# Kernel tuning notes

Hardware: AMD Instinct MI355X
Metric: run time of the kernel (lower is better)

The kernel has to match this reference:

```python
import jax, jax.numpy as jnp
import numpy as np

B, L, HID = 256, 4096, 128
INNER = 8
LR = 0.01  # INFERENCE_LR


def setup_inputs() -> dict:
    key = jax.random.key(0)
    k_h, k_w1, k_b1, k_w2, k_b2 = jax.random.split(key, 5)
    bound1 = 1.0 / np.sqrt(HID)
    bound2 = 1.0 / np.sqrt(INNER)
    return {
        "h": jax.random.normal(k_h, (B, L, HID), dtype=jnp.float32),
        "W1": jax.random.uniform(k_w1, (INNER, HID), jnp.float32, -bound1, bound1),
        "b1": jax.random.uniform(k_b1, (INNER,), jnp.float32, -bound1, bound1),
        "W2": jax.random.uniform(k_w2, (HID, INNER), jnp.float32, -bound2, bound2),
        "b2": jax.random.uniform(k_b2, (HID,), jnp.float32, -bound2, bound2),
    }


def reference(h, W1, b1, W2, b2):
    Bsz, Ls, H = h.shape
    ts = jnp.arange(0, Ls - 3, 2)  # SGD step positions (static)
    inv_h = 2.0 / H  # d(mean sq err)/d(pred) factor over H elements

    def per_batch(hb):  # hb: (L, H)
        ks = hb[ts]       # keys  h[b, t]
        vs = hb[ts + 1]   # values h[b, t+1]

        def step(carry, kv):
            w1, c1, w2, c2 = carry
            k, v = kv
            a = w1 @ k + c1                 # (inner,)
            r = jnp.maximum(a, 0.0)
            pred = w2 @ r + c2              # (H,)
            g = inv_h * (pred - v)          # dLoss/dpred
            dW2 = jnp.outer(g, r)
            db2 = g
            da = (w2.T @ g) * (a > 0)
            dW1 = jnp.outer(da, k)
            db1 = da
            return (w1 - LR * dW1, c1 - LR * db1,
                    w2 - LR * dW2, c2 - LR * db2), None

        (w1, c1, w2, c2), _ = jax.lax.scan(step, (W1, b1, W2, b2), (ks, vs))
        x = hb[-1]
        return w2 @ jnp.maximum(w1 @ x + c1, 0.0) + c2  # (H,)

    return jax.vmap(per_batch)(h)  # (B, H)
```

## Files before the change

kernel.cpp:

```cpp
#include <hip/hip_runtime.h>

#define LRC 0.01f
#define LSEQ 4096
#define HIDDIM 128

typedef float f32x2 __attribute__((ext_vector_type(2)));
typedef unsigned int u32x2 __attribute__((ext_vector_type(2)));

#define RL(x, L) __int_as_float(__builtin_amdgcn_readlane(__float_as_int(x), (L)))
#define RORADD(x, ctrl)                                                      \
  x += __int_as_float(__builtin_amdgcn_update_dpp(                           \
      0, __float_as_int(x), (ctrl), 0xf, 0xf, true))

__device__ __forceinline__ float allred4(float x0, float x1, float x2,
                                         float x3) {
  u32x2 s1 = __builtin_amdgcn_permlane32_swap(__float_as_uint(x0),
                                              __float_as_uint(x1), false, false);
  float z01 = __uint_as_float(s1.x) + __uint_as_float(s1.y);
  u32x2 s2 = __builtin_amdgcn_permlane32_swap(__float_as_uint(x2),
                                              __float_as_uint(x3), false, false);
  float z23 = __uint_as_float(s2.x) + __uint_as_float(s2.y);
  u32x2 s3 = __builtin_amdgcn_permlane16_swap(__float_as_uint(z01),
                                              __float_as_uint(z23), false, false);
  float y = __uint_as_float(s3.x) + __uint_as_float(s3.y);
  RORADD(y, 0x128); RORADD(y, 0x124); RORADD(y, 0x122); RORADD(y, 0x121);
  return y;
}

__device__ __forceinline__ float allred1(float x) {
  u32x2 s1 = __builtin_amdgcn_permlane32_swap(__float_as_uint(x),
                                              __float_as_uint(x), false, false);
  float z = __uint_as_float(s1.x) + __uint_as_float(s1.y);
  u32x2 s2 = __builtin_amdgcn_permlane16_swap(__float_as_uint(z),
                                              __float_as_uint(z), false, false);
  z = __uint_as_float(s2.x) + __uint_as_float(s2.y);
  RORADD(z, 0x128); RORADD(z, 0x124); RORADD(z, 0x122); RORADD(z, 0x121);
  return z;
}

#define BAR() asm volatile("s_waitcnt lgkmcnt(0)\n\ts_barrier" ::: "memory")

__global__ __launch_bounds__(128) void ttt_kernel(
    const float* __restrict__ h, const float* __restrict__ W1,
    const float* __restrict__ b1, const float* __restrict__ W2,
    const float* __restrict__ b2, float* __restrict__ out) {
  __shared__ __align__(16) float sm[80];
  const int b = blockIdx.x;
  const int tid = threadIdx.x;
  const int wv = tid >> 6;
  const int lane = tid & 63;
  const int g = lane >> 4;
  const int sig = ((g & 1) << 1) | (g >> 1);
  const int d0 = lane * 2;
  const float* __restrict__ hb = h + (size_t)b * (LSEQ * HIDDIM);

  if (wv == 0) {
    const float cneg = -(LRC * 2.0f / (float)HIDDIM);
    f32x2 w2v[8];
#pragma unroll
    for (int i = 0; i < 8; ++i) {
      w2v[i].x = W2[(size_t)d0 * 8 + i];
      w2v[i].y = W2[(size_t)(d0 + 1) * 8 + i];
    }
    f32x2 b2v = *(const f32x2*)(b2 + d0);
    float b1A = b1[sig], b1B = b1[4 + sig];
    f32x2 vS0 = *(const f32x2*)(hb + 1 * HIDDIM + d0);
    f32x2 vS1 = *(const f32x2*)(hb + 3 * HIDDIM + d0);
    f32x2 vS2 = *(const f32x2*)(hb + 5 * HIDDIM + d0);
    f32x2 vS3 = *(const f32x2*)(hb + 7 * HIDDIM + d0);
    float pGlx = 0.0f, pGly = 0.0f;
    float pR0 = 0, pR1 = 0, pR2 = 0, pR3 = 0, pR4 = 0, pR5 = 0, pR6 = 0,
          pR7 = 0;
    float dm2A = 0, dm2B = 0, dm1A = 0, dm1B = 0;

    BAR();

    auto CORE = [&](float aA, float aB, f32x2 vcur, float& daAo, float& daBo,
                    bool defer) {
      float rA = fmaxf(aA, 0.0f), rB = fmaxf(aB, 0.0f);
      float r0 = RL(rA, 0), r1 = RL(rA, 32), r2 = RL(rA, 16), r3 = RL(rA, 48);
      float r4 = RL(rB, 0), r5 = RL(rB, 32), r6 = RL(rB, 16), r7 = RL(rB, 48);
      float px0 = fmaf(w2v[0].x, r0, b2v.x), py0 = fmaf(w2v[0].y, r0, b2v.y);
      float px1 = w2v[1].x * r1, py1 = w2v[1].y * r1;
      px0 = fmaf(w2v[2].x, r2, px0); py0 = fmaf(w2v[2].y, r2, py0);
      px1 = fmaf(w2v[3].x, r3, px1); py1 = fmaf(w2v[3].y, r3, py1);
      px0 = fmaf(w2v[4].x, r4, px0); py0 = fmaf(w2v[4].y, r4, py0);
      px1 = fmaf(w2v[5].x, r5, px1); py1 = fmaf(w2v[5].y, r5, py1);
      px0 = fmaf(w2v[6].x, r6, px0); py0 = fmaf(w2v[6].y, r6, py0);
      px1 = fmaf(w2v[7].x, r7, px1); py1 = fmaf(w2v[7].y, r7, py1);
      float glx = (px0 + px1 - vcur.x) * cneg;
      float gly = (py0 + py1 - vcur.y) * cneg;
      float dp[8];
#pragma unroll
      for (int i = 0; i < 8; ++i) dp[i] = fmaf(w2v[i].x, glx, w2v[i].y * gly);
      float zA = allred4(dp[0], dp[1], dp[2], dp[3]);
      float zB = allred4(dp[4], dp[5], dp[6], dp[7]);
      daAo = (aA > 0.0f) ? zA : 0.0f;
      daBo = (aB > 0.0f) ? zB : 0.0f;
      if (!defer) {
        w2v[0].x = fmaf(glx, r0, w2v[0].x); w2v[0].y = fmaf(gly, r0, w2v[0].y);
        w2v[1].x = fmaf(glx, r1, w2v[1].x); w2v[1].y = fmaf(gly, r1, w2v[1].y);
        w2v[2].x = fmaf(glx, r2, w2v[2].x); w2v[2].y = fmaf(gly, r2, w2v[2].y);
        w2v[3].x = fmaf(glx, r3, w2v[3].x); w2v[3].y = fmaf(gly, r3, w2v[3].y);
        w2v[4].x = fmaf(glx, r4, w2v[4].x); w2v[4].y = fmaf(gly, r4, w2v[4].y);
        w2v[5].x = fmaf(glx, r5, w2v[5].x); w2v[5].y = fmaf(gly, r5, w2v[5].y);
        w2v[6].x = fmaf(glx, r6, w2v[6].x); w2v[6].y = fmaf(gly, r6, w2v[6].y);
        w2v[7].x = fmaf(glx, r7, w2v[7].x); w2v[7].y = fmaf(gly, r7, w2v[7].y);
        b2v.x += glx;
        b2v.y += gly;
      } else {
        pGlx = glx; pGly = gly;
        pR0 = r0; pR1 = r1; pR2 = r2; pR3 = r3;
        pR4 = r4; pR5 = r5; pR6 = r6; pR7 = r7;
      }
    };

    auto APPLY_PEND = [&]() {
      w2v[0].x = fmaf(pGlx, pR0, w2v[0].x); w2v[0].y = fmaf(pGly, pR0, w2v[0].y);
      w2v[1].x = fmaf(pGlx, pR1, w2v[1].x); w2v[1].y = fmaf(pGly, pR1, w2v[1].y);
      w2v[2].x = fmaf(pGlx, pR2, w2v[2].x); w2v[2].y = fmaf(pGly, pR2, w2v[2].y);
      w2v[3].x = fmaf(pGlx, pR3, w2v[3].x); w2v[3].y = fmaf(pGly, pR3, w2v[3].y);
      w2v[4].x = fmaf(pGlx, pR4, w2v[4].x); w2v[4].y = fmaf(pGly, pR4, w2v[4].y);
      w2v[5].x = fmaf(pGlx, pR5, w2v[5].x); w2v[5].y = fmaf(pGly, pR5, w2v[5].y);
      w2v[6].x = fmaf(pGlx, pR6, w2v[6].x); w2v[6].y = fmaf(pGly, pR6, w2v[6].y);
      w2v[7].x = fmaf(pGlx, pR7, w2v[7].x); w2v[7].y = fmaf(pGly, pR7, w2v[7].y);
      b2v.x += pGlx;
      b2v.y += pGly;
    };

    auto EPA = [&](int ep, int e) {
      const int tpo = ep * 16, kko = 32 + ep * 5, dao = 48 + ep * 16;
      int rv0 = 4 * e + 9;  if (rv0 > 4095) rv0 = 4095;
      int rv1 = 4 * e + 11; if (rv1 > 4095) rv1 = 4095;
      f32x2 vI0 = *(const f32x2*)(hb + (size_t)rv0 * HIDDIM + d0);
      f32x2 vI1 = *(const f32x2*)(hb + (size_t)rv1 * HIDDIM + d0);
      float tpPA = sm[tpo + sig], tpPB = sm[tpo + 4 + sig];
      float tpQA = sm[tpo + 8 + sig], tpQB = sm[tpo + 12 + sig];
      float kk1 = sm[kko], kk2 = sm[kko + 1], kk3 = sm[kko + 2],
            kk4 = sm[kko + 3], kk5 = sm[kko + 4];
      APPLY_PEND();
      float aA = fmaf(dm2A, kk1, fmaf(dm1A, kk2, tpPA + b1A));
      float aB = fmaf(dm2B, kk1, fmaf(dm1B, kk2, tpPB + b1B));
      float daPA, daPB;
      CORE(aA, aB, vS0, daPA, daPB, false);
      if ((lane & 15) == 0) { sm[dao + sig] = daPA; sm[dao + 4 + sig] = daPB; }
      b1A += daPA;
      b1B += daPB;
      float aQA = fmaf(dm2A, kk3, fmaf(dm1A, kk4, fmaf(daPA, kk5, tpQA + b1A)));
      float aQB = fmaf(dm2B, kk3, fmaf(dm1B, kk4, fmaf(daPB, kk5, tpQB + b1B)));
      float daQA, daQB;
      CORE(aQA, aQB, vS1, daQA, daQB, true);
      if ((lane & 15) == 0) { sm[dao + 8 + sig] = daQA; sm[dao + 12 + sig] = daQB; }
      b1A += daQA;
      b1B += daQB;
      dm2A = daPA; dm2B = daPB;
      dm1A = daQA; dm1B = daQB;
      vS0 = vS2; vS1 = vS3; vS2 = vI0; vS3 = vI1;
      BAR();
    };

    for (int pr = 0; pr < 511; ++pr) {
      EPA(0, 2 * pr);
      EPA(1, 2 * pr + 1);
    }
    EPA(0, 1022);
    {
      float tpPA = sm[16 + sig], tpPB = sm[20 + sig];
      float tpQA = sm[24 + sig], tpQB = sm[28 + sig];
      float kk1 = sm[37], kk2 = sm[38], kk3 = sm[39], kk4 = sm[40],
            kk5 = sm[41];
      APPLY_PEND();
      float aA = fmaf(dm2A, kk1, fmaf(dm1A, kk2, tpPA + b1A));
      float aB = fmaf(dm2B, kk1, fmaf(dm1B, kk2, tpPB + b1B));
      float daA, daB;
      CORE(aA, aB, vS0, daA, daB, false);
      b1A += daA;
      b1B += daB;
      float fA = fmaf(dm2A, kk3, fmaf(dm1A, kk4, fmaf(daA, kk5, tpQA + b1A)));
      float fB = fmaf(dm2B, kk3, fmaf(dm1B, kk4, fmaf(daB, kk5, tpQB + b1B)));
      float rA = fmaxf(fA, 0.0f), rB = fmaxf(fB, 0.0f);
      float r0 = RL(rA, 0), r1 = RL(rA, 32), r2 = RL(rA, 16), r3 = RL(rA, 48);
      float r4 = RL(rB, 0), r5 = RL(rB, 32), r6 = RL(rB, 16), r7 = RL(rB, 48);
      float ox = fmaf(w2v[0].x, r0, b2v.x), oy = fmaf(w2v[0].y, r0, b2v.y);
      ox = fmaf(w2v[1].x, r1, ox); oy = fmaf(w2v[1].y, r1, oy);
      ox = fmaf(w2v[2].x, r2, ox); oy = fmaf(w2v[2].y, r2, oy);
      ox = fmaf(w2v[3].x, r3, ox); oy = fmaf(w2v[3].y, r3, oy);
      ox = fmaf(w2v[4].x, r4, ox); oy = fmaf(w2v[4].y, r4, oy);
      ox = fmaf(w2v[5].x, r5, ox); oy = fmaf(w2v[5].y, r5, oy);
      ox = fmaf(w2v[6].x, r6, ox); oy = fmaf(w2v[6].y, r6, oy);
      ox = fmaf(w2v[7].x, r7, ox); oy = fmaf(w2v[7].y, r7, oy);
      f32x2 o = {ox, oy};
      *(f32x2*)(out + (size_t)b * HIDDIM + d0) = o;
    }
  } else {
    f32x2 w1v[8];
#pragma unroll
    for (int i = 0; i < 8; ++i)
      w1v[i] = *(const f32x2*)(W1 + i * HIDDIM + d0);
    f32x2 kR2 = *(const f32x2*)(hb + 0 * HIDDIM + d0);
    f32x2 kR3 = *(const f32x2*)(hb + 2 * HIDDIM + d0);
    f32x2 kR4 = *(const f32x2*)(hb + 4 * HIDDIM + d0);
    f32x2 kR5 = *(const f32x2*)(hb + 6 * HIDDIM + d0);
    f32x2 kR0 = kR2, kR1 = kR2;
    f32x2 kI0 = *(const f32x2*)(hb + 8 * HIDDIM + d0);
    f32x2 kI1 = *(const f32x2*)(hb + 10 * HIDDIM + d0);
    if (lane < 16) sm[64 + lane] = 0.0f;
    {
      float pa[8], pb[8];
#pragma unroll
      for (int i = 0; i < 8; ++i) {
        pa[i] = fmaf(w1v[i].x, kR2.x, w1v[i].y * kR2.y);
        pb[i] = fmaf(w1v[i].x, kR3.x, w1v[i].y * kR3.y);
      }
      float zA = allred4(pa[0], pa[1], pa[2], pa[3]);
      float zB = allred4(pa[4], pa[5], pa[6], pa[7]);
      float tA = allred4(pb[0], pb[1], pb[2], pb[3]);
      float tB = allred4(pb[4], pb[5], pb[6], pb[7]);
      float kk01 = allred1(fmaf(kR2.x, kR3.x, kR2.y * kR3.y));
      if ((lane & 15) == 0) {
        sm[0 + sig] = zA;   sm[4 + sig] = zB;
        sm[8 + sig] = tA;   sm[12 + sig] = tB;
      }
      if (lane < 4) sm[32 + lane] = 0.0f;
      if (lane == 0) sm[36] = kk01;
    }
    BAR();

    auto EPB = [&](int ep, int e) {
      const int dao = 48 + (1 - ep) * 16;
      const int tpo = (1 - ep) * 16, kko = 32 + (1 - ep) * 5;
      int m6 = 2 * e + 6, m7 = 2 * e + 7;
      int r6 = (m6 >= 2047) ? 4095 : 2 * m6;
      int r7 = (m7 >= 2047) ? 4095 : 2 * m7;
      f32x2 kN0 = *(const f32x2*)(hb + (size_t)r6 * HIDDIM + d0);
      f32x2 kN1 = *(const f32x2*)(hb + (size_t)r7 * HIDDIM + d0);
      float4 qa = *(float4*)&sm[dao], qb = *(float4*)&sm[dao + 4];
      float4 qc = *(float4*)&sm[dao + 8], qd = *(float4*)&sm[dao + 12];
      float c1 = fmaf(kR2.x, kR4.x, kR2.y * kR4.y);
      float c2 = fmaf(kR3.x, kR4.x, kR3.y * kR4.y);
      float c3 = fmaf(kR2.x, kR5.x, kR2.y * kR5.y);
      float c4 = fmaf(kR3.x, kR5.x, kR3.y * kR5.y);
      float c5 = fmaf(kR4.x, kR5.x, kR4.y * kR5.y);
      float ykk = allred4(c1, c2, c3, c4);
      float yk5 = allred1(c5);
      float daP[8] = {qa.x, qa.y, qa.z, qa.w, qb.x, qb.y, qb.z, qb.w};
      float daQ[8] = {qc.x, qc.y, qc.z, qc.w, qd.x, qd.y, qd.z, qd.w};
#pragma unroll
      for (int i = 0; i < 8; ++i) {
        w1v[i].x = fmaf(daP[i], kR0.x, w1v[i].x);
        w1v[i].y = fmaf(daP[i], kR0.y, w1v[i].y);
      }
#pragma unroll
      for (int i = 0; i < 8; ++i) {
        w1v[i].x = fmaf(daQ[i], kR1.x, w1v[i].x);
        w1v[i].y = fmaf(daQ[i], kR1.y, w1v[i].y);
      }
      float tp[8], tq[8];
#pragma unroll
      for (int i = 0; i < 8; ++i) {
        tp[i] = fmaf(w1v[i].x, kR4.x, w1v[i].y * kR4.y);
        tq[i] = fmaf(w1v[i].x, kR5.x, w1v[i].y * kR5.y);
      }
      float tA = allred4(tp[0], tp[1], tp[2], tp[3]);
      float tB = allred4(tp[4], tp[5], tp[6], tp[7]);
      float uA = allred4(tq[0], tq[1], tq[2], tq[3]);
      float uB = allred4(tq[4], tq[5], tq[6], tq[7]);
      if ((lane & 15) == 0) {
        sm[tpo + sig] = tA;      sm[tpo + 4 + sig] = tB;
        sm[tpo + 8 + sig] = uA;  sm[tpo + 12 + sig] = uB;
        sm[kko + sig] = ykk;
      }
      if (lane == 0) sm[kko + 4] = yk5;
      kR0 = kR2; kR1 = kR3; kR2 = kR4; kR3 = kR5;
      kR4 = kI0; kR5 = kI1; kI0 = kN0; kI1 = kN1;
      BAR();
    };

    for (int pr = 0; pr < 511; ++pr) {
      EPB(0, 2 * pr);
      EPB(1, 2 * pr + 1);
    }
    EPB(0, 1022);
  }
}

extern "C" void kernel_launch(void* const* d_in, const int* in_sizes, int n_in,
                              void* d_out, int out_size, void* d_ws, size_t ws_size,
                              hipStream_t stream) {
  const float* h  = (const float*)d_in[0];
  const float* W1 = (const float*)d_in[1];
  const float* b1 = (const float*)d_in[2];
  const float* W2 = (const float*)d_in[3];
  const float* b2 = (const float*)d_in[4];
  float* out = (float*)d_out;
  ttt_kernel<<<256, 128, 0, stream>>>(h, W1, b1, W2, b2, out);
}
```

Before: 533.1 us.

## Process two batch sequences per workgroup with interleaved independent recurrences

Each workgroup now runs two batch elements (P and Q) side by side. Their independent serial SGD chains are interleaved in the same wavefronts to hide the latency of cross-lane reductions and readlane operations, and the grid is halved to 128 blocks. This trades fewer active CUs (128 of 256) and higher register pressure for more instruction-level parallelism per step. The shared-memory scratch doubles to hold both sequences' exchange buffers.

```diff
diff --git a/kernel.cpp b/kernel.cpp
--- a/kernel.cpp
+++ b/kernel.cpp
@@ -40,43 +40,57 @@
 
 #define BAR() asm volatile("s_waitcnt lgkmcnt(0)\n\ts_barrier" ::: "memory")
 
+__device__ __forceinline__ float dot2(f32x2 a, f32x2 b) {
+  return fmaf(a.x, b.x, a.y * b.y);
+}
+
+struct PendT {
+  float glx, gly, r0, r1, r2, r3, r4, r5, r6, r7;
+};
+
 __global__ __launch_bounds__(128) void ttt_kernel(
     const float* __restrict__ h, const float* __restrict__ W1,
     const float* __restrict__ b1, const float* __restrict__ W2,
     const float* __restrict__ b2, float* __restrict__ out) {
-  __shared__ __align__(16) float sm[80];
-  const int b = blockIdx.x;
+  __shared__ __align__(16) float sm[160];
+  const int bp = blockIdx.x * 2;
   const int tid = threadIdx.x;
   const int wv = tid >> 6;
   const int lane = tid & 63;
   const int g = lane >> 4;
   const int sig = ((g & 1) << 1) | (g >> 1);
   const int d0 = lane * 2;
-  const float* __restrict__ hb = h + (size_t)b * (LSEQ * HIDDIM);
+  const bool rowlead = ((lane & 15) == 0);
+  const float* __restrict__ hbP = h + (size_t)bp * (LSEQ * HIDDIM);
+  const float* __restrict__ hbQ = hbP + (size_t)LSEQ * HIDDIM;
 
   if (wv == 0) {
     const float cneg = -(LRC * 2.0f / (float)HIDDIM);
-    f32x2 w2v[8];
+    f32x2 w2P[8], w2Q[8];
 #pragma unroll
     for (int i = 0; i < 8; ++i) {
-      w2v[i].x = W2[(size_t)d0 * 8 + i];
-      w2v[i].y = W2[(size_t)(d0 + 1) * 8 + i];
-    }
-    f32x2 b2v = *(const f32x2*)(b2 + d0);
-    float b1A = b1[sig], b1B = b1[4 + sig];
-    f32x2 vS0 = *(const f32x2*)(hb + 1 * HIDDIM + d0);
-    f32x2 vS1 = *(const f32x2*)(hb + 3 * HIDDIM + d0);
-    f32x2 vS2 = *(const f32x2*)(hb + 5 * HIDDIM + d0);
-    f32x2 vS3 = *(const f32x2*)(hb + 7 * HIDDIM + d0);
-    float pGlx = 0.0f, pGly = 0.0f;
-    float pR0 = 0, pR1 = 0, pR2 = 0, pR3 = 0, pR4 = 0, pR5 = 0, pR6 = 0,
-          pR7 = 0;
-    float dm2A = 0, dm2B = 0, dm1A = 0, dm1B = 0;
-
-    BAR();
-
-    auto CORE = [&](float aA, float aB, f32x2 vcur, float& daAo, float& daBo,
-                    bool defer) {
+      f32x2 t;
+      t.x = W2[(size_t)d0 * 8 + i];
+      t.y = W2[(size_t)(d0 + 1) * 8 + i];
+      w2P[i] = t;
+      w2Q[i] = t;
+    }
+    f32x2 b2c = *(const f32x2*)(b2 + d0);
+    f32x2 b2P = b2c, b2Q = b2c;
+    float b1AP = b1[sig], b1BP = b1[4 + sig];
+    float b1AQ = b1AP, b1BQ = b1BP;
+    f32x2 vP[4], vQ[4];
+#pragma unroll
+    for (int x = 0; x < 4; ++x) {
+      vP[x] = *(const f32x2*)(hbP + (size_t)(2 * x + 1) * HIDDIM + d0);
+      vQ[x] = *(const f32x2*)(hbQ + (size_t)(2 * x + 1) * HIDDIM + d0);
+    }
+    PendT pdP = {}, pdQ = {};
+    float dm2AP = 0, dm2BP = 0, dm1AP = 0, dm1BP = 0;
+    float dm2AQ = 0, dm2BQ = 0, dm1AQ = 0, dm1BQ = 0;
+
+    auto CORE = [&](f32x2(&w2v)[8], f32x2& b2v, float aA, float aB, f32x2 vcur,
+                    float& daAo, float& daBo, PendT& pd, bool defer) {
       float rA = fmaxf(aA, 0.0f), rB = fmaxf(aB, 0.0f);
       float r0 = RL(rA, 0), r1 = RL(rA, 32), r2 = RL(rA, 16), r3 = RL(rA, 48);
       float r4 = RL(rB, 0), r5 = RL(rB, 32), r6 = RL(rB, 16), r7 = RL(rB, 48);
@@ -109,53 +123,84 @@
         b2v.x += glx;
         b2v.y += gly;
       } else {
-        pGlx = glx; pGly = gly;
-        pR0 = r0; pR1 = r1; pR2 = r2; pR3 = r3;
-        pR4 = r4; pR5 = r5; pR6 = r6; pR7 = r7;
+        pd.glx = glx; pd.gly = gly;
+        pd.r0 = r0; pd.r1 = r1; pd.r2 = r2; pd.r3 = r3;
+        pd.r4 = r4; pd.r5 = r5; pd.r6 = r6; pd.r7 = r7;
       }
     };
-
-    auto APPLY_PEND = [&]() {
-      w2v[0].x = fmaf(pGlx, pR0, w2v[0].x); w2v[0].y = fmaf(pGly, pR0, w2v[0].y);
-      w2v[1].x = fmaf(pGlx, pR1, w2v[1].x); w2v[1].y = fmaf(pGly, pR1, w2v[1].y);
-      w2v[2].x = fmaf(pGlx, pR2, w2v[2].x); w2v[2].y = fmaf(pGly, pR2, w2v[2].y);
-      w2v[3].x = fmaf(pGlx, pR3, w2v[3].x); w2v[3].y = fmaf(pGly, pR3, w2v[3].y);
-      w2v[4].x = fmaf(pGlx, pR4, w2v[4].x); w2v[4].y = fmaf(pGly, pR4, w2v[4].y);
-      w2v[5].x = fmaf(pGlx, pR5, w2v[5].x); w2v[5].y = fmaf(pGly, pR5, w2v[5].y);
-      w2v[6].x = fmaf(pGlx, pR6, w2v[6].x); w2v[6].y = fmaf(pGly, pR6, w2v[6].y);
-      w2v[7].x = fmaf(pGlx, pR7, w2v[7].x); w2v[7].y = fmaf(pGly, pR7, w2v[7].y);
-      b2v.x += pGlx;
-      b2v.y += pGly;
+    auto PEND = [&](f32x2(&w2v)[8], f32x2& b2v, PendT& pd) {
+      w2v[0].x = fmaf(pd.glx, pd.r0, w2v[0].x);
+      w2v[0].y = fmaf(pd.gly, pd.r0, w2v[0].y);
+      w2v[1].x = fmaf(pd.glx, pd.r1, w2v[1].x);
+      w2v[1].y = fmaf(pd.gly, pd.r1, w2v[1].y);
+      w2v[2].x = fmaf(pd.glx, pd.r2, w2v[2].x);
+      w2v[2].y = fmaf(pd.gly, pd.r2, w2v[2].y);
+      w2v[3].x = fmaf(pd.glx, pd.r3, w2v[3].x);
+      w2v[3].y = fmaf(pd.gly, pd.r3, w2v[3].y);
+      w2v[4].x = fmaf(pd.glx, pd.r4, w2v[4].x);
+      w2v[4].y = fmaf(pd.gly, pd.r4, w2v[4].y);
+      w2v[5].x = fmaf(pd.glx, pd.r5, w2v[5].x);
+      w2v[5].y = fmaf(pd.gly, pd.r5, w2v[5].y);
+      w2v[6].x = fmaf(pd.glx, pd.r6, w2v[6].x);
+      w2v[6].y = fmaf(pd.gly, pd.r6, w2v[6].y);
+      w2v[7].x = fmaf(pd.glx, pd.r7, w2v[7].x);
+      w2v[7].y = fmaf(pd.gly, pd.r7, w2v[7].y);
+      b2v.x += pd.glx;
+      b2v.y += pd.gly;
     };
+
+    BAR();
 
     auto EPA = [&](int ep, int e) {
       const int tpo = ep * 16, kko = 32 + ep * 5, dao = 48 + ep * 16;
+      float t0AP = sm[tpo + sig], t0BP = sm[tpo + 4 + sig];
+      float t1AP = sm[tpo + 8 + sig], t1BP = sm[tpo + 12 + sig];
+      float k1P = sm[kko], k2P = sm[kko + 1], k3P = sm[kko + 2],
+            k4P = sm[kko + 3], k5P = sm[kko + 4];
+      float t0AQ = sm[80 + tpo + sig], t0BQ = sm[80 + tpo + 4 + sig];
+      float t1AQ = sm[80 + tpo + 8 + sig], t1BQ = sm[80 + tpo + 12 + sig];
+      float k1Q = sm[80 + kko], k2Q = sm[80 + kko + 1], k3Q = sm[80 + kko + 2],
+            k4Q = sm[80 + kko + 3], k5Q = sm[80 + kko + 4];
       int rv0 = 4 * e + 9;  if (rv0 > 4095) rv0 = 4095;
       int rv1 = 4 * e + 11; if (rv1 > 4095) rv1 = 4095;
-      f32x2 vI0 = *(const f32x2*)(hb + (size_t)rv0 * HIDDIM + d0);
-      f32x2 vI1 = *(const f32x2*)(hb + (size_t)rv1 * HIDDIM + d0);
-      float tpPA = sm[tpo + sig], tpPB = sm[tpo + 4 + sig];
-      float tpQA = sm[tpo + 8 + sig], tpQB = sm[tpo + 12 + sig];
-      float kk1 = sm[kko], kk2 = sm[kko + 1], kk3 = sm[kko + 2],
-            kk4 = sm[kko + 3], kk5 = sm[kko + 4];
-      APPLY_PEND();
-      float aA = fmaf(dm2A, kk1, fmaf(dm1A, kk2, tpPA + b1A));
-      float aB = fmaf(dm2B, kk1, fmaf(dm1B, kk2, tpPB + b1B));
-      float daPA, daPB;
-      CORE(aA, aB, vS0, daPA, daPB, false);
-      if ((lane & 15) == 0) { sm[dao + sig] = daPA; sm[dao + 4 + sig] = daPB; }
-      b1A += daPA;
-      b1B += daPB;
-      float aQA = fmaf(dm2A, kk3, fmaf(dm1A, kk4, fmaf(daPA, kk5, tpQA + b1A)));
-      float aQB = fmaf(dm2B, kk3, fmaf(dm1B, kk4, fmaf(daPB, kk5, tpQB + b1B)));
-      float daQA, daQB;
-      CORE(aQA, aQB, vS1, daQA, daQB, true);
-      if ((lane & 15) == 0) { sm[dao + 8 + sig] = daQA; sm[dao + 12 + sig] = daQB; }
-      b1A += daQA;
-      b1B += daQB;
-      dm2A = daPA; dm2B = daPB;
-      dm1A = daQA; dm1B = daQB;
-      vS0 = vS2; vS1 = vS3; vS2 = vI0; vS3 = vI1;
+      f32x2 iP0 = *(const f32x2*)(hbP + (size_t)rv0 * HIDDIM + d0);
+      f32x2 iP1 = *(const f32x2*)(hbP + (size_t)rv1 * HIDDIM + d0);
+      f32x2 iQ0 = *(const f32x2*)(hbQ + (size_t)rv0 * HIDDIM + d0);
+      f32x2 iQ1 = *(const f32x2*)(hbQ + (size_t)rv1 * HIDDIM + d0);
+      PEND(w2P, b2P, pdP);
+      PEND(w2Q, b2Q, pdQ);
+      float aAP = fmaf(dm2AP, k1P, fmaf(dm1AP, k2P, t0AP + b1AP));
+      float aBP = fmaf(dm2BP, k1P, fmaf(dm1BP, k2P, t0BP + b1BP));
+      float aAQ = fmaf(dm2AQ, k1Q, fmaf(dm1AQ, k2Q, t0AQ + b1AQ));
+      float aBQ = fmaf(dm2BQ, k1Q, fmaf(dm1BQ, k2Q, t0BQ + b1BQ));
+      float dPAP, dPBP, dPAQ, dPBQ;
+      CORE(w2P, b2P, aAP, aBP, vP[0], dPAP, dPBP, pdP, false);
+      CORE(w2Q, b2Q, aAQ, aBQ, vQ[0], dPAQ, dPBQ, pdQ, false);
+      if (rowlead) {
+        sm[dao + sig] = dPAP;      sm[dao + 4 + sig] = dPBP;
+        sm[80 + dao + sig] = dPAQ; sm[80 + dao + 4 + sig] = dPBQ;
+      }
+      b1AP += dPAP; b1BP += dPBP; b1AQ += dPAQ; b1BQ += dPBQ;
+      float a2AP = fmaf(dm2AP, k3P, fmaf(dm1AP, k4P,
+                   fmaf(dPAP, k5P, t1AP + b1AP)));
+      float a2BP = fmaf(dm2BP, k3P, fmaf(dm1BP, k4P,
+                   fmaf(dPBP, k5P, t1BP + b1BP)));
+      float a2AQ = fmaf(dm2AQ, k3Q, fmaf(dm1AQ, k4Q,
+                   fmaf(dPAQ, k5Q, t1AQ + b1AQ)));
+      float a2BQ = fmaf(dm2BQ, k3Q, fmaf(dm1BQ, k4Q,
+                   fmaf(dPBQ, k5Q, t1BQ + b1BQ)));
+      float dQAP, dQBP, dQAQ, dQBQ;
+      CORE(w2P, b2P, a2AP, a2BP, vP[1], dQAP, dQBP, pdP, true);
+      CORE(w2Q, b2Q, a2AQ, a2BQ, vQ[1], dQAQ, dQBQ, pdQ, true);
+      if (rowlead) {
+        sm[dao + 8 + sig] = dQAP;      sm[dao + 12 + sig] = dQBP;
+        sm[80 + dao + 8 + sig] = dQAQ; sm[80 + dao + 12 + sig] = dQBQ;
+      }
+      b1AP += dQAP; b1BP += dQBP; b1AQ += dQAQ; b1BQ += dQBQ;
+      dm2AP = dPAP; dm2BP = dPBP; dm1AP = dQAP; dm1BP = dQBP;
+      dm2AQ = dPAQ; dm2BQ = dPBQ; dm1AQ = dQAQ; dm1BQ = dQBQ;
+      vP[0] = vP[2]; vP[1] = vP[3]; vP[2] = iP0; vP[3] = iP1;
+      vQ[0] = vQ[2]; vQ[1] = vQ[3]; vQ[2] = iQ0; vQ[3] = iQ1;
       BAR();
     };
 
@@ -165,64 +210,126 @@
     }
     EPA(0, 1022);
     {
-      float tpPA = sm[16 + sig], tpPB = sm[20 + sig];
-      float tpQA = sm[24 + sig], tpQB = sm[28 + sig];
-      float kk1 = sm[37], kk2 = sm[38], kk3 = sm[39], kk4 = sm[40],
-            kk5 = sm[41];
-      APPLY_PEND();
-      float aA = fmaf(dm2A, kk1, fmaf(dm1A, kk2, tpPA + b1A));
-      float aB = fmaf(dm2B, kk1, fmaf(dm1B, kk2, tpPB + b1B));
-      float daA, daB;
-      CORE(aA, aB, vS0, daA, daB, false);
-      b1A += daA;
-      b1B += daB;
-      float fA = fmaf(dm2A, kk3, fmaf(dm1A, kk4, fmaf(daA, kk5, tpQA + b1A)));
-      float fB = fmaf(dm2B, kk3, fmaf(dm1B, kk4, fmaf(daB, kk5, tpQB + b1B)));
-      float rA = fmaxf(fA, 0.0f), rB = fmaxf(fB, 0.0f);
-      float r0 = RL(rA, 0), r1 = RL(rA, 32), r2 = RL(rA, 16), r3 = RL(rA, 48);
-      float r4 = RL(rB, 0), r5 = RL(rB, 32), r6 = RL(rB, 16), r7 = RL(rB, 48);
-      float ox = fmaf(w2v[0].x, r0, b2v.x), oy = fmaf(w2v[0].y, r0, b2v.y);
-      ox = fmaf(w2v[1].x, r1, ox); oy = fmaf(w2v[1].y, r1, oy);
-      ox = fmaf(w2v[2].x, r2, ox); oy = fmaf(w2v[2].y, r2, oy);
-      ox = fmaf(w2v[3].x, r3, ox); oy = fmaf(w2v[3].y, r3, oy);
-      ox = fmaf(w2v[4].x, r4, ox); oy = fmaf(w2v[4].y, r4, oy);
-      ox = fmaf(w2v[5].x, r5, ox); oy = fmaf(w2v[5].y, r5, oy);
-      ox = fmaf(w2v[6].x, r6, ox); oy = fmaf(w2v[6].y, r6, oy);
-      ox = fmaf(w2v[7].x, r7, ox); oy = fmaf(w2v[7].y, r7, oy);
-      f32x2 o = {ox, oy};
-      *(f32x2*)(out + (size_t)b * HIDDIM + d0) = o;
+      float t0AP = sm[16 + sig], t0BP = sm[20 + sig];
+      float t1AP = sm[24 + sig], t1BP = sm[28 + sig];
+      float k1P = sm[37], k2P = sm[38], k3P = sm[39], k4P = sm[40],
+            k5P = sm[41];
+      float t0AQ = sm[96 + sig], t0BQ = sm[100 + sig];
+      float t1AQ = sm[104 + sig], t1BQ = sm[108 + sig];
+      float k1Q = sm[117], k2Q = sm[118], k3Q = sm[119], k4Q = sm[120],
+            k5Q = sm[121];
+      PEND(w2P, b2P, pdP);
+      PEND(w2Q, b2Q, pdQ);
+      float aAP = fmaf(dm2AP, k1P, fmaf(dm1AP, k2P, t0AP + b1AP));
+      float aBP = fmaf(dm2BP, k1P, fmaf(dm1BP, k2P, t0BP + b1BP));
+      float aAQ = fmaf(dm2AQ, k1Q, fmaf(dm1AQ, k2Q, t0AQ + b1AQ));
+      float aBQ = fmaf(dm2BQ, k1Q, fmaf(dm1BQ, k2Q, t0BQ + b1BQ));
+      float dAP, dBP, dAQ, dBQ;
+      CORE(w2P, b2P, aAP, aBP, vP[0], dAP, dBP, pdP, false);
+      CORE(w2Q, b2Q, aAQ, aBQ, vQ[0], dAQ, dBQ, pdQ, false);
+      b1AP += dAP; b1BP += dBP; b1AQ += dAQ; b1BQ += dBQ;
+      float fAP = fmaf(dm2AP, k3P, fmaf(dm1AP, k4P,
+                  fmaf(dAP, k5P, t1AP + b1AP)));
+      float fBP = fmaf(dm2BP, k3P, fmaf(dm1BP, k4P,
+                  fmaf(dBP, k5P, t1BP + b1BP)));
+      float fAQ = fmaf(dm2AQ, k3Q, fmaf(dm1AQ, k4Q,
+                  fmaf(dAQ, k5Q, t1AQ + b1AQ)));
+      float fBQ = fmaf(dm2BQ, k3Q, fmaf(dm1BQ, k4Q,
+                  fmaf(dBQ, k5Q, t1BQ + b1BQ)));
+      {
+        float rA = fmaxf(fAP, 0.0f), rB = fmaxf(fBP, 0.0f);
+        float r0 = RL(rA, 0), r1 = RL(rA, 32), r2 = RL(rA, 16), r3 = RL(rA, 48);
+        float r4 = RL(rB, 0), r5 = RL(rB, 32), r6 = RL(rB, 16), r7 = RL(rB, 48);
+        float ox = fmaf(w2P[0].x, r0, b2P.x), oy = fmaf(w2P[0].y, r0, b2P.y);
+        ox = fmaf(w2P[1].x, r1, ox); oy = fmaf(w2P[1].y, r1, oy);
+        ox = fmaf(w2P[2].x, r2, ox); oy = fmaf(w2P[2].y, r2, oy);
+        ox = fmaf(w2P[3].x, r3, ox); oy = fmaf(w2P[3].y, r3, oy);
+        ox = fmaf(w2P[4].x, r4, ox); oy = fmaf(w2P[4].y, r4, oy);
+        ox = fmaf(w2P[5].x, r5, ox); oy = fmaf(w2P[5].y, r5, oy);
+        ox = fmaf(w2P[6].x, r6, ox); oy = fmaf(w2P[6].y, r6, oy);
+        ox = fmaf(w2P[7].x, r7, ox); oy = fmaf(w2P[7].y, r7, oy);
+        f32x2 o = {ox, oy};
+        *(f32x2*)(out + (size_t)bp * HIDDIM + d0) = o;
+      }
+      {
+        float rA = fmaxf(fAQ, 0.0f), rB = fmaxf(fBQ, 0.0f);
+        float r0 = RL(rA, 0), r1 = RL(rA, 32), r2 = RL(rA, 16), r3 = RL(rA, 48);
+        float r4 = RL(rB, 0), r5 = RL(rB, 32), r6 = RL(rB, 16), r7 = RL(rB, 48);
+        float ox = fmaf(w2Q[0].x, r0, b2Q.x), oy = fmaf(w2Q[0].y, r0, b2Q.y);
+        ox = fmaf(w2Q[1].x, r1, ox); oy = fmaf(w2Q[1].y, r1, oy);
+        ox = fmaf(w2Q[2].x, r2, ox); oy = fmaf(w2Q[2].y, r2, oy);
+        ox = fmaf(w2Q[3].x, r3, ox); oy = fmaf(w2Q[3].y, r3, oy);
+        ox = fmaf(w2Q[4].x, r4, ox); oy = fmaf(w2Q[4].y, r4, oy);
+        ox = fmaf(w2Q[5].x, r5, ox); oy = fmaf(w2Q[5].y, r5, oy);
+        ox = fmaf(w2Q[6].x, r6, ox); oy = fmaf(w2Q[6].y, r6, oy);
+        ox = fmaf(w2Q[7].x, r7, ox); oy = fmaf(w2Q[7].y, r7, oy);
+        f32x2 o = {ox, oy};
+        *(f32x2*)(out + (size_t)(bp + 1) * HIDDIM + d0) = o;
+      }
     }
   } else {
-    f32x2 w1v[8];
-#pragma unroll
-    for (int i = 0; i < 8; ++i)
-      w1v[i] = *(const f32x2*)(W1 + i * HIDDIM + d0);
-    f32x2 kR2 = *(const f32x2*)(hb + 0 * HIDDIM + d0);
-    f32x2 kR3 = *(const f32x2*)(hb + 2 * HIDDIM + d0);
-    f32x2 kR4 = *(const f32x2*)(hb + 4 * HIDDIM + d0);
-    f32x2 kR5 = *(const f32x2*)(hb + 6 * HIDDIM + d0);
-    f32x2 kR0 = kR2, kR1 = kR2;
-    f32x2 kI0 = *(const f32x2*)(hb + 8 * HIDDIM + d0);
-    f32x2 kI1 = *(const f32x2*)(hb + 10 * HIDDIM + d0);
-    if (lane < 16) sm[64 + lane] = 0.0f;
+    f32x2 w1P[8], w1Q[8];
+#pragma unroll
+    for (int i = 0; i < 8; ++i) {
+      f32x2 t = *(const f32x2*)(W1 + i * HIDDIM + d0);
+      w1P[i] = t;
+      w1Q[i] = t;
+    }
+    f32x2 kRP[6], kRQ[6], kIP0, kIP1, kIQ0, kIQ1;
+    kRP[2] = *(const f32x2*)(hbP + 0 * HIDDIM + d0);
+    kRP[3] = *(const f32x2*)(hbP + 2 * HIDDIM + d0);
+    kRP[4] = *(const f32x2*)(hbP + 4 * HIDDIM + d0);
+    kRP[5] = *(const f32x2*)(hbP + 6 * HIDDIM + d0);
+    kIP0 = *(const f32x2*)(hbP + 8 * HIDDIM + d0);
+    kIP1 = *(const f32x2*)(hbP + 10 * HIDDIM + d0);
+    kRP[0] = kRP[2]; kRP[1] = kRP[2];
+    kRQ[2] = *(const f32x2*)(hbQ + 0 * HIDDIM + d0);
+    kRQ[3] = *(const f32x2*)(hbQ + 2 * HIDDIM + d0);
+    kRQ[4] = *(const f32x2*)(hbQ + 4 * HIDDIM + d0);
+    kRQ[5] = *(const f32x2*)(hbQ + 6 * HIDDIM + d0);
+    kIQ0 = *(const f32x2*)(hbQ + 8 * HIDDIM + d0);
+    kIQ1 = *(const f32x2*)(hbQ + 10 * HIDDIM + d0);
+    kRQ[0] = kRQ[2]; kRQ[1] = kRQ[2];
+    if (lane < 16) {
+      sm[64 + lane] = 0.0f;
+      sm[144 + lane] = 0.0f;
+    }
     {
       float pa[8], pb[8];
 #pragma unroll
       for (int i = 0; i < 8; ++i) {
-        pa[i] = fmaf(w1v[i].x, kR2.x, w1v[i].y * kR2.y);
-        pb[i] = fmaf(w1v[i].x, kR3.x, w1v[i].y * kR3.y);
+        pa[i] = dot2(w1P[i], kRP[2]);
+        pb[i] = dot2(w1P[i], kRP[3]);
       }
       float zA = allred4(pa[0], pa[1], pa[2], pa[3]);
       float zB = allred4(pa[4], pa[5], pa[6], pa[7]);
       float tA = allred4(pb[0], pb[1], pb[2], pb[3]);
       float tB = allred4(pb[4], pb[5], pb[6], pb[7]);
-      float kk01 = allred1(fmaf(kR2.x, kR3.x, kR2.y * kR3.y));
-      if ((lane & 15) == 0) {
-        sm[0 + sig] = zA;   sm[4 + sig] = zB;
-        sm[8 + sig] = tA;   sm[12 + sig] = tB;
-      }
-      if (lane < 4) sm[32 + lane] = 0.0f;
-      if (lane == 0) sm[36] = kk01;
+      float kk01P = allred1(dot2(kRP[2], kRP[3]));
+#pragma unroll
+      for (int i = 0; i < 8; ++i) {
+        pa[i] = dot2(w1Q[i], kRQ[2]);
+        pb[i] = dot2(w1Q[i], kRQ[3]);
+      }
+      float zAq = allred4(pa[0], pa[1], pa[2], pa[3]);
+      float zBq = allred4(pa[4], pa[5], pa[6], pa[7]);
+      float tAq = allred4(pb[0], pb[1], pb[2], pb[3]);
+      float tBq = allred4(pb[4], pb[5], pb[6], pb[7]);
+      float kk01Q = allred1(dot2(kRQ[2], kRQ[3]));
+      if (rowlead) {
+        sm[0 + sig] = zA;       sm[4 + sig] = zB;
+        sm[8 + sig] = tA;       sm[12 + sig] = tB;
+        sm[80 + 0 + sig] = zAq; sm[80 + 4 + sig] = zBq;
+        sm[80 + 8 + sig] = tAq; sm[80 + 12 + sig] = tBq;
+      }
+      if (lane < 4) {
+        sm[32 + lane] = 0.0f;
+        sm[112 + lane] = 0.0f;
+      }
+      if (lane == 0) {
+        sm[36] = kk01P;
+        sm[116] = kk01Q;
+      }
     }
     BAR();
 
@@ -232,47 +339,74 @@
       int m6 = 2 * e + 6, m7 = 2 * e + 7;
       int r6 = (m6 >= 2047) ? 4095 : 2 * m6;
       int r7 = (m7 >= 2047) ? 4095 : 2 * m7;
-      f32x2 kN0 = *(const f32x2*)(hb + (size_t)r6 * HIDDIM + d0);
-      f32x2 kN1 = *(const f32x2*)(hb + (size_t)r7 * HIDDIM + d0);
-      float4 qa = *(float4*)&sm[dao], qb = *(float4*)&sm[dao + 4];
-      float4 qc = *(float4*)&sm[dao + 8], qd = *(float4*)&sm[dao + 12];
-      float c1 = fmaf(kR2.x, kR4.x, kR2.y * kR4.y);
-      float c2 = fmaf(kR3.x, kR4.x, kR3.y * kR4.y);
-      float c3 = fmaf(kR2.x, kR5.x, kR2.y * kR5.y);
-      float c4 = fmaf(kR3.x, kR5.x, kR3.y * kR5.y);
-      float c5 = fmaf(kR4.x, kR5.x, kR4.y * kR5.y);
-      float ykk = allred4(c1, c2, c3, c4);
-      float yk5 = allred1(c5);
-      float daP[8] = {qa.x, qa.y, qa.z, qa.w, qb.x, qb.y, qb.z, qb.w};
-      float daQ[8] = {qc.x, qc.y, qc.z, qc.w, qd.x, qd.y, qd.z, qd.w};
+      f32x2 nP0 = *(const f32x2*)(hbP + (size_t)r6 * HIDDIM + d0);
+      f32x2 nP1 = *(const f32x2*)(hbP + (size_t)r7 * HIDDIM + d0);
+      f32x2 nQ0 = *(const f32x2*)(hbQ + (size_t)r6 * HIDDIM + d0);
+      f32x2 nQ1 = *(const f32x2*)(hbQ + (size_t)r7 * HIDDIM + d0);
+      float4 p0 = *(float4*)&sm[dao], p1 = *(float4*)&sm[dao + 4];
+      float4 p2 = *(float4*)&sm[dao + 8], p3 = *(float4*)&sm[dao + 12];
+      float4 q0 = *(float4*)&sm[80 + dao], q1 = *(float4*)&sm[80 + dao + 4];
+      float4 q2 = *(float4*)&sm[80 + dao + 8], q3 = *(float4*)&sm[80 + dao + 12];
+      float c1P = dot2(kRP[2], kRP[4]), c2P = dot2(kRP[3], kRP[4]);
+      float c3P = dot2(kRP[2], kRP[5]), c4P = dot2(kRP[3], kRP[5]);
+      float c5P = dot2(kRP[4], kRP[5]);
+      float c1Q = dot2(kRQ[2], kRQ[4]), c2Q = dot2(kRQ[3], kRQ[4]);
+      float c3Q = dot2(kRQ[2], kRQ[5]), c4Q = dot2(kRQ[3], kRQ[5]);
+      float c5Q = dot2(kRQ[4], kRQ[5]);
+      float ykP = allred4(c1P, c2P, c3P, c4P);
+      float y5P = allred1(c5P);
+      float ykQ = allred4(c1Q, c2Q, c3Q, c4Q);
+      float y5Q = allred1(c5Q);
+      if (rowlead) {
+        sm[kko + sig] = ykP;
+        sm[80 + kko + sig] = ykQ;
+      }
+      if (lane == 0) {
+        sm[kko + 4] = y5P;
+        sm[80 + kko + 4] = y5Q;
+      }
+      float dPa[8] = {p0.x, p0.y, p0.z, p0.w, p1.x, p1.y, p1.z, p1.w};
+      float dPb[8] = {p2.x, p2.y, p2.z, p2.w, p3.x, p3.y, p3.z, p3.w};
+      float dQa[8] = {q0.x, q0.y, q0.z, q0.w, q1.x, q1.y, q1.z, q1.w};
+      float dQb[8] = {q2.x, q2.y, q2.z, q2.w, q3.x, q3.y, q3.z, q3.w};
 #pragma unroll
       for (int i = 0; i < 8; ++i) {
-        w1v[i].x = fmaf(daP[i], kR0.x, w1v[i].x);
-        w1v[i].y = fmaf(daP[i], kR0.y, w1v[i].y);
-      }
-#pragma unroll
-      for (int i = 0; i < 8; ++i) {
-        w1v[i].x = fmaf(daQ[i], kR1.x, w1v[i].x);
-        w1v[i].y = fmaf(daQ[i], kR1.y, w1v[i].y);
-      }
-      float tp[8], tq[8];
-#pragma unroll
-      for (int i = 0; i < 8; ++i) {
-        tp[i] = fmaf(w1v[i].x, kR4.x, w1v[i].y * kR4.y);
-        tq[i] = fmaf(w1v[i].x, kR5.x, w1v[i].y * kR5.y);
-      }
-      float tA = allred4(tp[0], tp[1], tp[2], tp[3]);
-      float tB = allred4(tp[4], tp[5], tp[6], tp[7]);
-      float uA = allred4(tq[0], tq[1], tq[2], tq[3]);
-      float uB = allred4(tq[4], tq[5], tq[6], tq[7]);
-      if ((lane & 15) == 0) {
-        sm[tpo + sig] = tA;      sm[tpo + 4 + sig] = tB;
-        sm[tpo + 8 + sig] = uA;  sm[tpo + 12 + sig] = uB;
-        sm[kko + sig] = ykk;
-      }
-      if (lane == 0) sm[kko + 4] = yk5;
-      kR0 = kR2; kR1 = kR3; kR2 = kR4; kR3 = kR5;
-      kR4 = kI0; kR5 = kI1; kI0 = kN0; kI1 = kN1;
+        w1P[i].x = fmaf(dPa[i], kRP[0].x, w1P[i].x);
+        w1P[i].y = fmaf(dPa[i], kRP[0].y, w1P[i].y);
+        w1P[i].x = fmaf(dPb[i], kRP[1].x, w1P[i].x);
+        w1P[i].y = fmaf(dPb[i], kRP[1].y, w1P[i].y);
+        w1Q[i].x = fmaf(dQa[i], kRQ[0].x, w1Q[i].x);
+        w1Q[i].y = fmaf(dQa[i], kRQ[0].y, w1Q[i].y);
+        w1Q[i].x = fmaf(dQb[i], kRQ[1].x, w1Q[i].x);
+        w1Q[i].y = fmaf(dQb[i], kRQ[1].y, w1Q[i].y);
+      }
+      float tp[8];
+#pragma unroll
+      for (int i = 0; i < 8; ++i) tp[i] = dot2(w1P[i], kRP[4]);
+      float tAP = allred4(tp[0], tp[1], tp[2], tp[3]);
+      float tBP = allred4(tp[4], tp[5], tp[6], tp[7]);
+#pragma unroll
+      for (int i = 0; i < 8; ++i) tp[i] = dot2(w1P[i], kRP[5]);
+      float uAP = allred4(tp[0], tp[1], tp[2], tp[3]);
+      float uBP = allred4(tp[4], tp[5], tp[6], tp[7]);
+#pragma unroll
+      for (int i = 0; i < 8; ++i) tp[i] = dot2(w1Q[i], kRQ[4]);
+      float tAQ = allred4(tp[0], tp[1], tp[2], tp[3]);
+      float tBQ = allred4(tp[4], tp[5], tp[6], tp[7]);
+#pragma unroll
+      for (int i = 0; i < 8; ++i) tp[i] = dot2(w1Q[i], kRQ[5]);
+      float uAQ = allred4(tp[0], tp[1], tp[2], tp[3]);
+      float uBQ = allred4(tp[4], tp[5], tp[6], tp[7]);
+      if (rowlead) {
+        sm[tpo + sig] = tAP;           sm[tpo + 4 + sig] = tBP;
+        sm[tpo + 8 + sig] = uAP;       sm[tpo + 12 + sig] = uBP;
+        sm[80 + tpo + sig] = tAQ;      sm[80 + tpo + 4 + sig] = tBQ;
+        sm[80 + tpo + 8 + sig] = uAQ;  sm[80 + tpo + 12 + sig] = uBQ;
+      }
+      kRP[0] = kRP[2]; kRP[1] = kRP[3]; kRP[2] = kRP[4]; kRP[3] = kRP[5];
+      kRP[4] = kIP0;   kRP[5] = kIP1;   kIP0 = nP0;      kIP1 = nP1;
+      kRQ[0] = kRQ[2]; kRQ[1] = kRQ[3]; kRQ[2] = kRQ[4]; kRQ[3] = kRQ[5];
+      kRQ[4] = kIQ0;   kRQ[5] = kIQ1;   kIQ0 = nQ0;      kIQ1 = nQ1;
       BAR();
     };
 
@@ -293,5 +427,5 @@
   const float* W2 = (const float*)d_in[3];
   const float* b2 = (const float*)d_in[4];
   float* out = (float*)d_out;
-  ttt_kernel<<<256, 128, 0, stream>>>(h, W1, b1, W2, b2, out);
+  ttt_kernel<<<128, 128, 0, stream>>>(h, W1, b1, W2, b2, out);
 }
```

Result: slower. 908.3 us (+70.4%).

## Replace per-step block barriers with shared-memory flag handshakes between waves

Applied to the files above, without the earlier changes.

Swaps the s_barrier that joined the two waves at every epoch for volatile LDS progress flags: each wave publishes its epoch counter and spin-waits only on the counter it actually depends on. The W1 wave can now run up to an epoch ahead of the W2 wave, so the two serial chains are less tightly lock-stepped, and the W1 wave computes its key-key dot products before it waits. The cost is spin-loop polling on LDS and reliance on LDS ordering and s_waitcnt for correctness, with a risk of races if the double-buffer slots are overwritten before they are read.

```diff
diff --git a/kernel.cpp b/kernel.cpp
--- a/kernel.cpp
+++ b/kernel.cpp
@@ -38,21 +38,32 @@
   return z;
 }
 
-#define BAR() asm volatile("s_waitcnt lgkmcnt(0)\n\ts_barrier" ::: "memory")
+__device__ __forceinline__ float dot2(f32x2 a, f32x2 b) {
+  return fmaf(a.x, b.x, a.y * b.y);
+}
 
 __global__ __launch_bounds__(128) void ttt_kernel(
     const float* __restrict__ h, const float* __restrict__ W1,
     const float* __restrict__ b1, const float* __restrict__ W2,
     const float* __restrict__ b2, float* __restrict__ out) {
   __shared__ __align__(16) float sm[80];
-  const int b = blockIdx.x;
+  __shared__ int flg[2];
+  volatile int* vf = flg;
+  const int bq = blockIdx.x;
   const int tid = threadIdx.x;
   const int wv = tid >> 6;
   const int lane = tid & 63;
   const int g = lane >> 4;
   const int sig = ((g & 1) << 1) | (g >> 1);
   const int d0 = lane * 2;
-  const float* __restrict__ hb = h + (size_t)b * (LSEQ * HIDDIM);
+  const bool rowlead = ((lane & 15) == 0);
+  const float* __restrict__ hb = h + (size_t)bq * (LSEQ * HIDDIM);
+
+  if (tid == 0) {
+    flg[0] = -1;
+    flg[1] = -1;
+  }
+  __syncthreads();
 
   if (wv == 0) {
     const float cneg = -(LRC * 2.0f / (float)HIDDIM);
@@ -64,16 +75,14 @@
     }
     f32x2 b2v = *(const f32x2*)(b2 + d0);
     float b1A = b1[sig], b1B = b1[4 + sig];
-    f32x2 vS0 = *(const f32x2*)(hb + 1 * HIDDIM + d0);
-    f32x2 vS1 = *(const f32x2*)(hb + 3 * HIDDIM + d0);
-    f32x2 vS2 = *(const f32x2*)(hb + 5 * HIDDIM + d0);
-    f32x2 vS3 = *(const f32x2*)(hb + 7 * HIDDIM + d0);
+    f32x2 vS[4];
+#pragma unroll
+    for (int x = 0; x < 4; ++x)
+      vS[x] = *(const f32x2*)(hb + (size_t)(2 * x + 1) * HIDDIM + d0);
     float pGlx = 0.0f, pGly = 0.0f;
     float pR0 = 0, pR1 = 0, pR2 = 0, pR3 = 0, pR4 = 0, pR5 = 0, pR6 = 0,
           pR7 = 0;
     float dm2A = 0, dm2B = 0, dm1A = 0, dm1B = 0;
-
-    BAR();
 
     auto CORE = [&](float aA, float aB, f32x2 vcur, float& daAo, float& daBo,
                     bool defer) {
@@ -114,7 +123,6 @@
         pR4 = r4; pR5 = r5; pR6 = r6; pR7 = r7;
       }
     };
-
     auto APPLY_PEND = [&]() {
       w2v[0].x = fmaf(pGlx, pR0, w2v[0].x); w2v[0].y = fmaf(pGly, pR0, w2v[0].y);
       w2v[1].x = fmaf(pGlx, pR1, w2v[1].x); w2v[1].y = fmaf(pGly, pR1, w2v[1].y);
@@ -128,12 +136,15 @@
       b2v.y += pGly;
     };
 
-    auto EPA = [&](int ep, int e) {
+    auto EPA = [&](int e) {
+      const int ep = e & 1;
       const int tpo = ep * 16, kko = 32 + ep * 5, dao = 48 + ep * 16;
       int rv0 = 4 * e + 9;  if (rv0 > 4095) rv0 = 4095;
       int rv1 = 4 * e + 11; if (rv1 > 4095) rv1 = 4095;
       f32x2 vI0 = *(const f32x2*)(hb + (size_t)rv0 * HIDDIM + d0);
       f32x2 vI1 = *(const f32x2*)(hb + (size_t)rv1 * HIDDIM + d0);
+      while (vf[1] < e) {}
+      asm volatile("" ::: "memory");
       float tpPA = sm[tpo + sig], tpPB = sm[tpo + 4 + sig];
       float tpQA = sm[tpo + 8 + sig], tpQB = sm[tpo + 12 + sig];
       float kk1 = sm[kko], kk2 = sm[kko + 1], kk3 = sm[kko + 2],
@@ -142,29 +153,28 @@
       float aA = fmaf(dm2A, kk1, fmaf(dm1A, kk2, tpPA + b1A));
       float aB = fmaf(dm2B, kk1, fmaf(dm1B, kk2, tpPB + b1B));
       float daPA, daPB;
-      CORE(aA, aB, vS0, daPA, daPB, false);
-      if ((lane & 15) == 0) { sm[dao + sig] = daPA; sm[dao + 4 + sig] = daPB; }
+      CORE(aA, aB, vS[0], daPA, daPB, false);
+      if (rowlead) { sm[dao + sig] = daPA; sm[dao + 4 + sig] = daPB; }
       b1A += daPA;
       b1B += daPB;
       float aQA = fmaf(dm2A, kk3, fmaf(dm1A, kk4, fmaf(daPA, kk5, tpQA + b1A)));
       float aQB = fmaf(dm2B, kk3, fmaf(dm1B, kk4, fmaf(daPB, kk5, tpQB + b1B)));
       float daQA, daQB;
-      CORE(aQA, aQB, vS1, daQA, daQB, true);
-      if ((lane & 15) == 0) { sm[dao + 8 + sig] = daQA; sm[dao + 12 + sig] = daQB; }
+      CORE(aQA, aQB, vS[1], daQA, daQB, true);
+      if (rowlead) { sm[dao + 8 + sig] = daQA; sm[dao + 12 + sig] = daQB; }
       b1A += daQA;
       b1B += daQB;
       dm2A = daPA; dm2B = daPB;
       dm1A = daQA; dm1B = daQB;
-      vS0 = vS2; vS1 = vS3; vS2 = vI0; vS3 = vI1;
-      BAR();
+      vS[0] = vS[2]; vS[1] = vS[3]; vS[2] = vI0; vS[3] = vI1;
+      asm volatile("s_waitcnt lgkmcnt(0)" ::: "memory");
+      if (lane == 0) vf[0] = e;
     };
 
-    for (int pr = 0; pr < 511; ++pr) {
-      EPA(0, 2 * pr);
-      EPA(1, 2 * pr + 1);
-    }
-    EPA(0, 1022);
+    for (int e = 0; e < 1023; ++e) EPA(e);
     {
+      while (vf[1] < 1023) {}
+      asm volatile("" ::: "memory");
       float tpPA = sm[16 + sig], tpPB = sm[20 + sig];
       float tpQA = sm[24 + sig], tpQB = sm[28 + sig];
       float kk1 = sm[37], kk2 = sm[38], kk3 = sm[39], kk4 = sm[40],
@@ -173,7 +183,7 @@
       float aA = fmaf(dm2A, kk1, fmaf(dm1A, kk2, tpPA + b1A));
       float aB = fmaf(dm2B, kk1, fmaf(dm1B, kk2, tpPB + b1B));
       float daA, daB;
-      CORE(aA, aB, vS0, daA, daB, false);
+      CORE(aA, aB, vS[0], daA, daB, false);
       b1A += daA;
       b1B += daB;
       float fA = fmaf(dm2A, kk3, fmaf(dm1A, kk4, fmaf(daA, kk5, tpQA + b1A)));
@@ -190,7 +200,7 @@
       ox = fmaf(w2v[6].x, r6, ox); oy = fmaf(w2v[6].y, r6, oy);
       ox = fmaf(w2v[7].x, r7, ox); oy = fmaf(w2v[7].y, r7, oy);
       f32x2 o = {ox, oy};
-      *(f32x2*)(out + (size_t)b * HIDDIM + d0) = o;
+      *(f32x2*)(out + (size_t)bq * HIDDIM + d0) = o;
     }
   } else {
     f32x2 w1v[8];
@@ -209,78 +219,73 @@
       float pa[8], pb[8];
 #pragma unroll
       for (int i = 0; i < 8; ++i) {
-        pa[i] = fmaf(w1v[i].x, kR2.x, w1v[i].y * kR2.y);
-        pb[i] = fmaf(w1v[i].x, kR3.x, w1v[i].y * kR3.y);
+        pa[i] = dot2(w1v[i], kR2);
+        pb[i] = dot2(w1v[i], kR3);
       }
       float zA = allred4(pa[0], pa[1], pa[2], pa[3]);
       float zB = allred4(pa[4], pa[5], pa[6], pa[7]);
       float tA = allred4(pb[0], pb[1], pb[2], pb[3]);
       float tB = allred4(pb[4], pb[5], pb[6], pb[7]);
-      float kk01 = allred1(fmaf(kR2.x, kR3.x, kR2.y * kR3.y));
-      if ((lane & 15) == 0) {
+      float kk01 = allred1(dot2(kR2, kR3));
+      if (rowlead) {
         sm[0 + sig] = zA;   sm[4 + sig] = zB;
         sm[8 + sig] = tA;   sm[12 + sig] = tB;
       }
       if (lane < 4) sm[32 + lane] = 0.0f;
       if (lane == 0) sm[36] = kk01;
     }
-    BAR();
-
-    auto EPB = [&](int ep, int e) {
+    asm volatile("s_waitcnt lgkmcnt(0)" ::: "memory");
+    if (lane == 0) vf[1] = 0;
+
+    auto EPB = [&](int f) {
+      const int ep = f & 1;
       const int dao = 48 + (1 - ep) * 16;
       const int tpo = (1 - ep) * 16, kko = 32 + (1 - ep) * 5;
-      int m6 = 2 * e + 6, m7 = 2 * e + 7;
+      int m6 = 2 * f + 6, m7 = 2 * f + 7;
       int r6 = (m6 >= 2047) ? 4095 : 2 * m6;
       int r7 = (m7 >= 2047) ? 4095 : 2 * m7;
       f32x2 kN0 = *(const f32x2*)(hb + (size_t)r6 * HIDDIM + d0);
       f32x2 kN1 = *(const f32x2*)(hb + (size_t)r7 * HIDDIM + d0);
-      float4 qa = *(float4*)&sm[dao], qb = *(float4*)&sm[dao + 4];
-      float4 qc = *(float4*)&sm[dao + 8], qd = *(float4*)&sm[dao + 12];
-      float c1 = fmaf(kR2.x, kR4.x, kR2.y * kR4.y);
-      float c2 = fmaf(kR3.x, kR4.x, kR3.y * kR4.y);
-      float c3 = fmaf(kR2.x, kR5.x, kR2.y * kR5.y);
-      float c4 = fmaf(kR3.x, kR5.x, kR3.y * kR5.y);
-      float c5 = fmaf(kR4.x, kR5.x, kR4.y * kR5.y);
+      float c1 = dot2(kR2, kR4), c2 = dot2(kR3, kR4);
+      float c3 = dot2(kR2, kR5), c4 = dot2(kR3, kR5);
+      float c5 = dot2(kR4, kR5);
       float ykk = allred4(c1, c2, c3, c4);
       float yk5 = allred1(c5);
-      float daP[8] = {qa.x, qa.y, qa.z, qa.w, qb.x, qb.y, qb.z, qb.w};
-      float daQ[8] = {qc.x, qc.y, qc.z, qc.w, qd.x, qd.y, qd.z, qd.w};
+      while (vf[0] < f - 1) {}
+      asm volatile("" ::: "memory");
+      float4 q0 = *(float4*)&sm[dao], q1 = *(float4*)&sm[dao + 4];
+      float4 q2 = *(float4*)&sm[dao + 8], q3 = *(float4*)&sm[dao + 12];
+      if (rowlead) sm[kko + sig] = ykk;
+      if (lane == 0) sm[kko + 4] = yk5;
+      float dP[8] = {q0.x, q0.y, q0.z, q0.w, q1.x, q1.y, q1.z, q1.w};
+      float dQ[8] = {q2.x, q2.y, q2.z, q2.w, q3.x, q3.y, q3.z, q3.w};
 #pragma unroll
       for (int i = 0; i < 8; ++i) {
-        w1v[i].x = fmaf(daP[i], kR0.x, w1v[i].x);
-        w1v[i].y = fmaf(daP[i], kR0.y, w1v[i].y);
-      }
-#pragma unroll
-      for (int i = 0; i < 8; ++i) {
-        w1v[i].x = fmaf(daQ[i], kR1.x, w1v[i].x);
-        w1v[i].y = fmaf(daQ[i], kR1.y, w1v[i].y);
-      }
-      float tp[8], tq[8];
-#pragma unroll
-      for (int i = 0; i < 8; ++i) {
-        tp[i] = fmaf(w1v[i].x, kR4.x, w1v[i].y * kR4.y);
-        tq[i] = fmaf(w1v[i].x, kR5.x, w1v[i].y * kR5.y);
-      }
+        w1v[i].x = fmaf(dP[i], kR0.x, w1v[i].x);
+        w1v[i].y = fmaf(dP[i], kR0.y, w1v[i].y);
+        w1v[i].x = fmaf(dQ[i], kR1.x, w1v[i].x);
+        w1v[i].y = fmaf(dQ[i], kR1.y, w1v[i].y);
+      }
+      float tp[8];
+#pragma unroll
+      for (int i = 0; i < 8; ++i) tp[i] = dot2(w1v[i], kR4);
       float tA = allred4(tp[0], tp[1], tp[2], tp[3]);
       float tB = allred4(tp[4], tp[5], tp[6], tp[7]);
-      float uA = allred4(tq[0], tq[1], tq[2], tq[3]);
-      float uB = allred4(tq[4], tq[5], tq[6], tq[7]);
-      if ((lane & 15) == 0) {
+#pragma unroll
+      for (int i = 0; i < 8; ++i) tp[i] = dot2(w1v[i], kR5);
+      float uA = allred4(tp[0], tp[1], tp[2], tp[3]);
+      float uB = allred4(tp[4], tp[5], tp[6], tp[7]);
+      if (rowlead) {
         sm[tpo + sig] = tA;      sm[tpo + 4 + sig] = tB;
         sm[tpo + 8 + sig] = uA;  sm[tpo + 12 + sig] = uB;
-        sm[kko + sig] = ykk;
-      }
-      if (lane == 0) sm[kko + 4] = yk5;
+      }
       kR0 = kR2; kR1 = kR3; kR2 = kR4; kR3 = kR5;
       kR4 = kI0; kR5 = kI1; kI0 = kN0; kI1 = kN1;
-      BAR();
+      asm volatile("s_waitcnt lgkmcnt(0)" ::: "memory");
+      if (lane == 0) vf[1] = f + 1;
     };
 
-    for (int pr = 0; pr < 511; ++pr) {
-      EPB(0, 2 * pr);
-      EPB(1, 2 * pr + 1);
-    }
-    EPB(0, 1022);
+    for (int f = 0; f < 1023; ++f) EPB(f);
   }
 }
 
```

Measured after the change: 1.022 ms. 91.7% more time.
